# Kernel tuning notes

Hardware: AMD Instinct MI355X
Metric: run time of the kernel (lower is better)

## Reference

```python
import jax, jax.numpy as jnp
import numpy as np

N_NODES = 100000
N_EDGES = 1600000
IN_FEAT = 512
HIDDEN = 128
N_CLASSES = 7


def gcn_conv(x, edge_index, edge_weight, W, b):
    """PyG GCNConv: add self-loops (weight 1), symmetric normalization, linear, scatter-add, bias."""
    n = x.shape[0]
    src = jnp.concatenate([edge_index[0], jnp.arange(n, dtype=edge_index.dtype)])
    dst = jnp.concatenate([edge_index[1], jnp.arange(n, dtype=edge_index.dtype)])
    w = jnp.concatenate([edge_weight, jnp.ones((n,), dtype=edge_weight.dtype)])
    deg = jax.ops.segment_sum(w, dst, num_segments=n)  # degree on destination (col)
    dinv = jnp.where(deg > 0, jax.lax.rsqrt(deg), 0.0)
    norm = dinv[src] * w * dinv[dst]                   # [E+N]
    h = x @ W                                          # [N, out] transform BEFORE propagate
    msg = h[src] * norm[:, None]                       # [E+N, out] irregular gather
    out = jax.ops.segment_sum(msg, dst, num_segments=n)  # scatter-reduce
    return out + b


def setup_inputs() -> dict:
    key = jax.random.key(0)
    k1, k2, k3, k4, k5, k6 = jax.random.split(key, 6)
    x = jax.random.normal(k1, (N_NODES, IN_FEAT), dtype=jnp.float32)
    edge_index = jax.random.randint(k2, (2, N_EDGES), 0, N_NODES, dtype=jnp.int32)
    edge_weight = jax.random.uniform(k3, (N_EDGES,), dtype=jnp.float32)
    s1 = 1.0 / np.sqrt(IN_FEAT)
    s2 = 1.0 / np.sqrt(HIDDEN)
    W1 = jax.random.uniform(k4, (IN_FEAT, HIDDEN), dtype=jnp.float32, minval=-s1, maxval=s1)
    b1 = jnp.zeros((HIDDEN,), dtype=jnp.float32)
    W2 = jax.random.uniform(k5, (HIDDEN, N_CLASSES), dtype=jnp.float32, minval=-s2, maxval=s2)
    b2 = jnp.zeros((N_CLASSES,), dtype=jnp.float32)
    return {"x": x, "edge_index": edge_index, "edge_weight": edge_weight,
            "W1": W1, "b1": b1, "W2": W2, "b2": b2}


def reference(x, edge_index, edge_weight, W1, b1, W2, b2):
    # eval mode: F.dropout(training=False) is identity
    h = jax.nn.elu(gcn_conv(x, edge_index, edge_weight, W1, b1))
    out = gcn_conv(h, edge_index, edge_weight, W2, b2)
    return jax.nn.log_softmax(out, axis=1)
```

## Files before the change

### kernel.cpp

```cpp
#include <hip/hip_runtime.h>
#include <hip/hip_bf16.h>
#include <math.h>

#define N_NODES 100000
#define N_EDGES 1600000
#define IN_F 512
#define HID 128
#define NCLS 7

#define DEG_SHIFT 43
#define DEG_WMASK ((1ull << 43) - 1)
#define DEG_SCALE 4194304.0f
#define DEG_INV_SCALE (1.0f / 4194304.0f)

typedef short short8 __attribute__((ext_vector_type(8)));
typedef float f32x4 __attribute__((ext_vector_type(4)));

__device__ __forceinline__ unsigned pack_bf16x2(float a, float b) {
  unsigned ua = __float_as_uint(a), ub = __float_as_uint(b);
  unsigned ra = (ua + 0x7FFFu + ((ua >> 16) & 1u)) >> 16;
  unsigned rb = (ub + 0x7FFFu + ((ub >> 16) & 1u)) >> 16;
  return ra | (rb << 16);
}
__device__ __forceinline__ unsigned short f32_to_bf16(float v) {
  unsigned u = __float_as_uint(v);
  return (unsigned short)((u + 0x7FFFu + ((u >> 16) & 1u)) >> 16);
}
__device__ __forceinline__ float bf_lo(unsigned u) { return __uint_as_float(u << 16); }
__device__ __forceinline__ float bf_hi(unsigned u) { return __uint_as_float(u & 0xFFFF0000u); }

__global__ void k_deg_count(const int* __restrict__ ei, const float* __restrict__ ew,
                            unsigned long long* __restrict__ packed, int* __restrict__ rank) {
  int e = blockIdx.x * blockDim.x + threadIdx.x;
  if (e >= N_EDGES) return;
  int d = ei[N_EDGES + e];
  unsigned long long fx = (unsigned long long)(ew[e] * DEG_SCALE + 0.5f);
  unsigned long long old = atomicAdd(&packed[d], (1ull << DEG_SHIFT) | fx);
  rank[e] = (int)(old >> DEG_SHIFT);
}

__global__ void k_dinv(const unsigned long long* __restrict__ packed,
                       float* __restrict__ dinv, int* __restrict__ cnt,
                       uint2* __restrict__ csr_pad) {
  int i = blockIdx.x * blockDim.x + threadIdx.x;
  if (i < 8) csr_pad[i] = make_uint2(0u, 0u);
  if (i >= N_NODES) return;
  unsigned long long p = packed[i];
  cnt[i] = (int)(p >> DEG_SHIFT);
  float wsum = (float)(p & DEG_WMASK) * DEG_INV_SCALE;
  dinv[i] = rsqrtf(wsum + 1.0f);
}

__global__ void k_w1t(const float* __restrict__ W1, uint4* __restrict__ w1bf) {
  int idx = blockIdx.x * 256 + threadIdx.x;
  int lane = idx & 63;
  int st = idx >> 6;
  int t = st & 7, s = st >> 3;
  int n = t * 16 + (lane & 15);
  int k0 = s * 32 + (lane >> 4) * 8;
  uint4 v;
  v.x = pack_bf16x2(W1[(size_t)(k0 + 0) * HID + n], W1[(size_t)(k0 + 1) * HID + n]);
  v.y = pack_bf16x2(W1[(size_t)(k0 + 2) * HID + n], W1[(size_t)(k0 + 3) * HID + n]);
  v.z = pack_bf16x2(W1[(size_t)(k0 + 4) * HID + n], W1[(size_t)(k0 + 5) * HID + n]);
  v.w = pack_bf16x2(W1[(size_t)(k0 + 6) * HID + n], W1[(size_t)(k0 + 7) * HID + n]);
  w1bf[idx] = v;
}

__global__ void k_scan_partial(const int* __restrict__ cnt, int* __restrict__ bsum) {
  __shared__ int s[256];
  int t = threadIdx.x;
  int base = blockIdx.x * 1024;
  int v = 0;
#pragma unroll
  for (int q = 0; q < 4; q++) {
    int idx = base + t * 4 + q;
    if (idx < N_NODES) v += cnt[idx];
  }
  s[t] = v;
  __syncthreads();
  for (int o = 128; o > 0; o >>= 1) {
    if (t < o) s[t] += s[t + o];
    __syncthreads();
  }
  if (t == 0) bsum[blockIdx.x] = s[0];
}

__global__ void k_scan_bsum(int* bsum, int nb) {
  if (threadIdx.x == 0 && blockIdx.x == 0) {
    int acc = 0;
    for (int i = 0; i < nb; i++) { int v = bsum[i]; bsum[i] = acc; acc += v; }
  }
}

__global__ void k_scan_final(const int* __restrict__ cnt, const int* __restrict__ bsum,
                             int* __restrict__ offs) {
  __shared__ int s[256];
  int t = threadIdx.x;
  int base = blockIdx.x * 1024;
  int v[4]; int sum = 0;
#pragma unroll
  for (int q = 0; q < 4; q++) {
    int idx = base + t * 4 + q;
    v[q] = (idx < N_NODES) ? cnt[idx] : 0;
    sum += v[q];
  }
  s[t] = sum;
  __syncthreads();
  for (int o = 1; o < 256; o <<= 1) {
    int x = (t >= o) ? s[t - o] : 0;
    __syncthreads();
    s[t] += x;
    __syncthreads();
  }
  int acc = s[t] - sum + bsum[blockIdx.x];
#pragma unroll
  for (int q = 0; q < 4; q++) {
    int idx = base + t * 4 + q;
    if (idx < N_NODES) offs[idx] = acc;
    acc += v[q];
  }
}

__global__ void k_fill(const int* __restrict__ ei, const float* __restrict__ ew,
                       const int* __restrict__ rank, const int* __restrict__ offs,
                       uint2* __restrict__ csr) {
  int e = blockIdx.x * blockDim.x + threadIdx.x;
  if (e >= N_EDGES) return;
  int sidx = ei[e];
  int d = ei[N_EDGES + e];
  int p = offs[d] + rank[e];
  csr[p] = make_uint2((unsigned)sidx, __float_as_uint(ew[e]));
}

#define SLABSTRIDE 132
__global__ __launch_bounds__(256) void k_gemm1(const float* __restrict__ x,
                                               const uint4* __restrict__ w1bf,
                                               const float* __restrict__ dinv,
                                               unsigned short* __restrict__ h_u16) {
  __shared__ unsigned slab[4 * 16 * SLABSTRIDE];
  const int tid = threadIdx.x;
  const int lane = tid & 63;
  const int wv = tid >> 6;
  const int gw = blockIdx.x * 4 + wv;
  if (gw >= N_NODES / 16) return;
  const int m0 = gw * 16;
  unsigned* ws = slab + wv * 16 * SLABSTRIDE;
  const int l16 = lane & 15, quad = lane >> 4;

  f32x4 acc[8];
#pragma unroll
  for (int t = 0; t < 8; t++) acc[t] = (f32x4){0.f, 0.f, 0.f, 0.f};

#pragma unroll
  for (int hf = 0; hf < 2; hf++) {
#pragma unroll
    for (int b = 0; b < 2; b++) {
      float4 v[8];
#pragma unroll
      for (int i = 0; i < 8; i++) {
        int row = b * 8 + i;
        v[i] = *(const float4*)(x + (size_t)(m0 + row) * IN_F + hf * 256 + lane * 4);
      }
#pragma unroll
      for (int i = 0; i < 8; i++) {
        int row = b * 8 + i;
        unsigned lo = pack_bf16x2(v[i].x, v[i].y);
        unsigned hi = pack_bf16x2(v[i].z, v[i].w);
        *(uint2*)&ws[row * SLABSTRIDE + lane * 2] = make_uint2(lo, hi);
      }
    }
    __threadfence_block();
#pragma unroll
    for (int ks = 0; ks < 8; ks++) {
      short8 af = *(const short8*)&ws[l16 * SLABSTRIDE + ks * 16 + quad * 4];
      const uint4* bbase = w1bf + (size_t)(hf * 8 + ks) * 8 * 64 + lane;
#pragma unroll
      for (int t = 0; t < 8; t++) {
        uint4 bv = bbase[t * 64];
        acc[t] = __builtin_amdgcn_mfma_f32_16x16x32_bf16(af, *(const short8*)&bv,
                                                         acc[t], 0, 0, 0);
      }
    }
  }
  float df[4];
#pragma unroll
  for (int r = 0; r < 4; r++) df[r] = dinv[m0 + quad * 4 + r];
#pragma unroll
  for (int t = 0; t < 8; t++)
#pragma unroll
    for (int r = 0; r < 4; r++)
      h_u16[(size_t)(m0 + quad * 4 + r) * HID + t * 16 + l16] = f32_to_bf16(acc[t][r] * df[r]);
}

__global__ __launch_bounds__(256) void k_agg1(const unsigned* __restrict__ h_u,
    const float* __restrict__ dinv, const int* __restrict__ offs, const int* __restrict__ cnt,
    const uint2* __restrict__ csr, const float* __restrict__ b1,
    unsigned* __restrict__ act1_u) {
  int i = blockIdx.x * 4 + (threadIdx.x >> 6);
  int lane = threadIdx.x & 63;
  if (i >= N_NODES) return;
  int start = offs[i], len = cnt[i];
  int end = start + len;
  float ax = 0.f, ay = 0.f;
  for (int p = start; p < end; p += 8) {
    uint2 e[8];
#pragma unroll
    for (int k = 0; k < 8; k++) e[k] = csr[p + k];
    unsigned u[8];
#pragma unroll
    for (int k = 0; k < 8; k++) u[k] = h_u[(size_t)e[k].x * 64 + lane];
#pragma unroll
    for (int k = 0; k < 8; k++) {
      float n = (k == 0 || p + k < end) ? __uint_as_float(e[k].y) : 0.f;
      ax = fmaf(bf_lo(u[k]), n, ax);
      ay = fmaf(bf_hi(u[k]), n, ay);
    }
  }
  float di = dinv[i];
  unsigned u = h_u[(size_t)i * 64 + lane];
  float2 bb = *(const float2*)(b1 + lane * 2);
  float vx = fmaf(di, ax + bf_lo(u), bb.x);
  float vy = fmaf(di, ay + bf_hi(u), bb.y);
  vx = vx > 0.f ? vx : expm1f(vx);
  vy = vy > 0.f ? vy : expm1f(vy);
  act1_u[(size_t)i * 64 + lane] = pack_bf16x2(vx, vy);
}

__global__ __launch_bounds__(256) void k_gemm2(const unsigned* __restrict__ act1_u,
                                               const float* __restrict__ W2,
                                               const float* __restrict__ dinv,
                                               float* __restrict__ h2) {
  __shared__ float sA[32][HID + 1];
  __shared__ float sW[HID * NCLS];
  const int tid = threadIdx.x;
  const int r0 = blockIdx.x * 32;
#pragma unroll
  for (int j = 0; j < 8; j++) {
    int idx = tid + j * 256;
    int row = idx >> 6;
    int c = idx & 63;
    unsigned u = act1_u[(size_t)(r0 + row) * 64 + c];
    sA[row][c * 2]     = bf_lo(u);
    sA[row][c * 2 + 1] = bf_hi(u);
  }
#pragma unroll
  for (int j = 0; j < 4; j++) {
    int idx = tid + j * 256;
    if (idx < HID * NCLS) sW[idx] = W2[idx];
  }
  __syncthreads();
  const int r = tid >> 3;
  const int c = tid & 7;
  float acc = 0.0f;
  if (c < NCLS) {
#pragma unroll 8
    for (int k = 0; k < HID; k++) acc = fmaf(sA[r][k], sW[k * NCLS + c], acc);
  }
  h2[(size_t)(r0 + r) * 8 + c] = acc * dinv[r0 + r];
}

__global__ __launch_bounds__(256) void k_agg2(const float* __restrict__ h2,
    const float* __restrict__ dinv, const int* __restrict__ offs, const int* __restrict__ cnt,
    const uint2* __restrict__ csr, const float* __restrict__ b2, float* __restrict__ out) {
  int tid = threadIdx.x;
  int i = blockIdx.x * 32 + (tid >> 3);
  int f = tid & 7;
  if (i >= N_NODES) return;
  int start = offs[i], len = cnt[i];
  int end = start + len;
  float acc = 0.0f;
  for (int p = start; p < end; p += 4) {
    uint2 e0 = csr[p];
    uint2 e1 = csr[p + 1];
    uint2 e2 = csr[p + 2];
    uint2 e3 = csr[p + 3];
    float v0 = h2[(size_t)e0.x * 8 + f];
    float v1 = h2[(size_t)e1.x * 8 + f];
    float v2 = h2[(size_t)e2.x * 8 + f];
    float v3 = h2[(size_t)e3.x * 8 + f];
    float n0 = __uint_as_float(e0.y);
    float n1 = (p + 1 < end) ? __uint_as_float(e1.y) : 0.f;
    float n2 = (p + 2 < end) ? __uint_as_float(e2.y) : 0.f;
    float n3 = (p + 3 < end) ? __uint_as_float(e3.y) : 0.f;
    acc = fmaf(v0, n0, acc);
    acc = fmaf(v1, n1, acc);
    acc = fmaf(v2, n2, acc);
    acc = fmaf(v3, n3, acc);
  }
  float di = dinv[i];
  float v = fmaf(di, acc + h2[(size_t)i * 8 + f], (f < NCLS) ? b2[f] : 0.0f);
  float vm = (f < NCLS) ? v : -INFINITY;
#pragma unroll
  for (int o = 1; o < 8; o <<= 1) vm = fmaxf(vm, __shfl_xor(vm, o, 8));
  float ex = (f < NCLS) ? expf(v - vm) : 0.0f;
  float s8 = ex;
#pragma unroll
  for (int o = 1; o < 8; o <<= 1) s8 += __shfl_xor(s8, o, 8);
  float lse = logf(s8);
  if (f < NCLS) out[(size_t)i * NCLS + f] = v - vm - lse;
}

extern "C" void kernel_launch(void* const* d_in, const int* in_sizes, int n_in,
                              void* d_out, int out_size, void* d_ws, size_t ws_size,
                              hipStream_t stream) {
  const float* x  = (const float*)d_in[0];
  const int*   ei = (const int*)d_in[1];
  const float* ew = (const float*)d_in[2];
  const float* W1 = (const float*)d_in[3];
  const float* b1 = (const float*)d_in[4];
  const float* W2 = (const float*)d_in[5];
  const float* b2 = (const float*)d_in[6];
  float* out = (float*)d_out;

  char* w = (char*)d_ws;
  const size_t Npad  = ((size_t)N_NODES * 4 + 255) & ~(size_t)255;
  const size_t Npad8 = ((size_t)N_NODES * 8 + 255) & ~(size_t)255;
  const size_t Epad  = ((size_t)N_EDGES * 4 + 255) & ~(size_t)255;
  size_t off = 0;
  unsigned long long* packed = (unsigned long long*)(w + off); off += Npad8;
  float*    dinv     = (float*)(w + off);    off += Npad;
  int*      cnt      = (int*)(w + off);      off += Npad;
  int*      offs     = (int*)(w + off);      off += Npad;
  int*      bsum     = (int*)(w + off);      off += 1024;
  int*      rank     = (int*)(w + off);      off += Epad;
  uint2*    csr      = (uint2*)(w + off);    off += ((size_t)(N_EDGES + 8) * 8 + 255) & ~(size_t)255;
  uint4*    w1bf     = (uint4*)(w + off);    off += (size_t)8192 * 16;
  unsigned short* h_u16 = (unsigned short*)(w + off); off += (size_t)N_NODES * HID * 2;
  unsigned* act1_u   = (unsigned*)(w + off); off += (size_t)N_NODES * 64 * 4;
  float*    h2       = (float*)(w + off);    off += (size_t)N_NODES * 8 * 4;

  hipMemsetAsync(packed, 0, Npad8, stream);

  k_deg_count<<<N_EDGES / 256, 256, 0, stream>>>(ei, ew, packed, rank);
  k_w1t<<<32, 256, 0, stream>>>(W1, w1bf);
  k_dinv<<<(N_NODES + 255) / 256, 256, 0, stream>>>(packed, dinv, cnt, csr + N_EDGES);
  const int nb = (N_NODES + 1023) / 1024;
  k_scan_partial<<<nb, 256, 0, stream>>>(cnt, bsum);
  k_scan_bsum<<<1, 64, 0, stream>>>(bsum, nb);
  k_scan_final<<<nb, 256, 0, stream>>>(cnt, bsum, offs);
  k_fill<<<N_EDGES / 256, 256, 0, stream>>>(ei, ew, rank, offs, csr);
  const int g1_waves = N_NODES / 16;
  k_gemm1<<<(g1_waves + 3) / 4, 256, 0, stream>>>(x, w1bf, dinv, h_u16);
  k_agg1<<<(N_NODES + 3) / 4, 256, 0, stream>>>((const unsigned*)h_u16, dinv, offs, cnt,
                                                csr, b1, act1_u);
  k_gemm2<<<N_NODES / 32, 256, 0, stream>>>(act1_u, W2, dinv, h2);
  k_agg2<<<N_NODES / 32, 256, 0, stream>>>(h2, dinv, offs, cnt, csr, b2, out);
}
```

Measured before the change: 550.1 us.

## Fuse setup kernels, fold gemm2 into agg1, simplify CSR fill and gemm1

Merges the dinv, W1 bf16 transpose and partial-scan kernels into one launch. Drops the per-edge rank array in favour of atomic cursor slots during the CSR fill, and reuses the advanced cursor as the row end. Folds the 128x7 second GEMM into the first aggregation epilogue using a wave-wide shuffle reduction, which removes the act1 round trip. gemm1 now loads A fragments straight from global memory instead of staging them in LDS. agg2 assigns one wave per node with edge-parallel lanes. The atomic fill makes CSR order nondeterministic, so float summation order varies between runs.

New measurement: 641.4 us. 16.6% more time.

```diff
diff --git a/kernel.cpp b/kernel.cpp
--- a/kernel.cpp
+++ b/kernel.cpp
@@ -1,5 +1,4 @@
 #include <hip/hip_runtime.h>
-#include <hip/hip_bf16.h>
 #include <math.h>
 
 #define N_NODES 100000
@@ -12,6 +11,7 @@
 #define DEG_WMASK ((1ull << 43) - 1)
 #define DEG_SCALE 4194304.0f
 #define DEG_INV_SCALE (1.0f / 4194304.0f)
+#define NB_SCAN 98
 
 typedef short short8 __attribute__((ext_vector_type(8)));
 typedef float f32x4 __attribute__((ext_vector_type(4)));
@@ -29,60 +29,56 @@
 __device__ __forceinline__ float bf_lo(unsigned u) { return __uint_as_float(u << 16); }
 __device__ __forceinline__ float bf_hi(unsigned u) { return __uint_as_float(u & 0xFFFF0000u); }
 
-__global__ void k_deg_count(const int* __restrict__ ei, const float* __restrict__ ew,
-                            unsigned long long* __restrict__ packed, int* __restrict__ rank) {
-  int e = blockIdx.x * blockDim.x + threadIdx.x;
-  if (e >= N_EDGES) return;
+__global__ void k_deg(const int* __restrict__ ei, const float* __restrict__ ew,
+                      unsigned long long* __restrict__ packed) {
+  int e = blockIdx.x * 256 + threadIdx.x;
   int d = ei[N_EDGES + e];
   unsigned long long fx = (unsigned long long)(ew[e] * DEG_SCALE + 0.5f);
-  unsigned long long old = atomicAdd(&packed[d], (1ull << DEG_SHIFT) | fx);
-  rank[e] = (int)(old >> DEG_SHIFT);
-}
-
-__global__ void k_dinv(const unsigned long long* __restrict__ packed,
-                       float* __restrict__ dinv, int* __restrict__ cnt,
-                       uint2* __restrict__ csr_pad) {
-  int i = blockIdx.x * blockDim.x + threadIdx.x;
-  if (i < 8) csr_pad[i] = make_uint2(0u, 0u);
-  if (i >= N_NODES) return;
-  unsigned long long p = packed[i];
-  cnt[i] = (int)(p >> DEG_SHIFT);
-  float wsum = (float)(p & DEG_WMASK) * DEG_INV_SCALE;
-  dinv[i] = rsqrtf(wsum + 1.0f);
-}
-
-__global__ void k_w1t(const float* __restrict__ W1, uint4* __restrict__ w1bf) {
-  int idx = blockIdx.x * 256 + threadIdx.x;
-  int lane = idx & 63;
-  int st = idx >> 6;
-  int t = st & 7, s = st >> 3;
-  int n = t * 16 + (lane & 15);
-  int k0 = s * 32 + (lane >> 4) * 8;
-  uint4 v;
-  v.x = pack_bf16x2(W1[(size_t)(k0 + 0) * HID + n], W1[(size_t)(k0 + 1) * HID + n]);
-  v.y = pack_bf16x2(W1[(size_t)(k0 + 2) * HID + n], W1[(size_t)(k0 + 3) * HID + n]);
-  v.z = pack_bf16x2(W1[(size_t)(k0 + 4) * HID + n], W1[(size_t)(k0 + 5) * HID + n]);
-  v.w = pack_bf16x2(W1[(size_t)(k0 + 6) * HID + n], W1[(size_t)(k0 + 7) * HID + n]);
-  w1bf[idx] = v;
-}
-
-__global__ void k_scan_partial(const int* __restrict__ cnt, int* __restrict__ bsum) {
-  __shared__ int s[256];
-  int t = threadIdx.x;
-  int base = blockIdx.x * 1024;
+  atomicAdd(&packed[d], (1ull << DEG_SHIFT) | fx);
+}
+
+__global__ void k_mid(const unsigned long long* __restrict__ packed,
+                      float* __restrict__ dinv, int* __restrict__ cnt, int* __restrict__ bsum,
+                      const float* __restrict__ W1, uint4* __restrict__ w1bf,
+                      uint2* __restrict__ csr_pad) {
+  const int b = blockIdx.x, t = threadIdx.x;
+  if (b >= NB_SCAN) {
+    int idx = (b - NB_SCAN) * 256 + t;
+    if (idx < 8) csr_pad[idx] = make_uint2(0u, 0u);
+    int lane = idx & 63;
+    int st = idx >> 6;
+    int tt = st & 7, ss = st >> 3;
+    int n = tt * 16 + (lane & 15);
+    int k0 = ss * 32 + (lane >> 4) * 8;
+    uint4 v;
+    v.x = pack_bf16x2(W1[(size_t)(k0 + 0) * HID + n], W1[(size_t)(k0 + 1) * HID + n]);
+    v.y = pack_bf16x2(W1[(size_t)(k0 + 2) * HID + n], W1[(size_t)(k0 + 3) * HID + n]);
+    v.z = pack_bf16x2(W1[(size_t)(k0 + 4) * HID + n], W1[(size_t)(k0 + 5) * HID + n]);
+    v.w = pack_bf16x2(W1[(size_t)(k0 + 6) * HID + n], W1[(size_t)(k0 + 7) * HID + n]);
+    w1bf[idx] = v;
+    return;
+  }
+  __shared__ int sh[256];
+  int base = b * 1024;
   int v = 0;
 #pragma unroll
   for (int q = 0; q < 4; q++) {
     int idx = base + t * 4 + q;
-    if (idx < N_NODES) v += cnt[idx];
-  }
-  s[t] = v;
+    if (idx < N_NODES) {
+      unsigned long long p = packed[idx];
+      int c = (int)(p >> DEG_SHIFT);
+      cnt[idx] = c;
+      dinv[idx] = rsqrtf((float)(p & DEG_WMASK) * DEG_INV_SCALE + 1.0f);
+      v += c;
+    }
+  }
+  sh[t] = v;
   __syncthreads();
   for (int o = 128; o > 0; o >>= 1) {
-    if (t < o) s[t] += s[t + o];
+    if (t < o) sh[t] += sh[t + o];
     __syncthreads();
   }
-  if (t == 0) bsum[blockIdx.x] = s[0];
+  if (t == 0) bsum[b] = sh[0];
 }
 
 __global__ void k_scan_bsum(int* bsum, int nb) {
@@ -93,7 +89,7 @@
 }
 
 __global__ void k_scan_final(const int* __restrict__ cnt, const int* __restrict__ bsum,
-                             int* __restrict__ offs) {
+                             int* __restrict__ offs, int* __restrict__ cursor) {
   __shared__ int s[256];
   int t = threadIdx.x;
   int base = blockIdx.x * 1024;
@@ -116,70 +112,54 @@
 #pragma unroll
   for (int q = 0; q < 4; q++) {
     int idx = base + t * 4 + q;
-    if (idx < N_NODES) offs[idx] = acc;
+    if (idx < N_NODES) { offs[idx] = acc; cursor[idx] = acc; }
     acc += v[q];
   }
 }
 
 __global__ void k_fill(const int* __restrict__ ei, const float* __restrict__ ew,
-                       const int* __restrict__ rank, const int* __restrict__ offs,
-                       uint2* __restrict__ csr) {
-  int e = blockIdx.x * blockDim.x + threadIdx.x;
-  if (e >= N_EDGES) return;
-  int sidx = ei[e];
+                       int* __restrict__ cursor, uint2* __restrict__ csr) {
+  int e = blockIdx.x * 256 + threadIdx.x;
+  int s = ei[e];
   int d = ei[N_EDGES + e];
-  int p = offs[d] + rank[e];
-  csr[p] = make_uint2((unsigned)sidx, __float_as_uint(ew[e]));
-}
-
-#define SLABSTRIDE 132
+  int p = atomicAdd(&cursor[d], 1);
+  csr[p] = make_uint2((unsigned)s, __float_as_uint(ew[e]));
+}
+
 __global__ __launch_bounds__(256) void k_gemm1(const float* __restrict__ x,
                                                const uint4* __restrict__ w1bf,
                                                const float* __restrict__ dinv,
                                                unsigned short* __restrict__ h_u16) {
-  __shared__ unsigned slab[4 * 16 * SLABSTRIDE];
   const int tid = threadIdx.x;
   const int lane = tid & 63;
   const int wv = tid >> 6;
   const int gw = blockIdx.x * 4 + wv;
   if (gw >= N_NODES / 16) return;
   const int m0 = gw * 16;
-  unsigned* ws = slab + wv * 16 * SLABSTRIDE;
   const int l16 = lane & 15, quad = lane >> 4;
+  const float* arow = x + (size_t)(m0 + l16) * IN_F + quad * 8;
 
   f32x4 acc[8];
 #pragma unroll
   for (int t = 0; t < 8; t++) acc[t] = (f32x4){0.f, 0.f, 0.f, 0.f};
 
 #pragma unroll
-  for (int hf = 0; hf < 2; hf++) {
-#pragma unroll
-    for (int b = 0; b < 2; b++) {
-      float4 v[8];
-#pragma unroll
-      for (int i = 0; i < 8; i++) {
-        int row = b * 8 + i;
-        v[i] = *(const float4*)(x + (size_t)(m0 + row) * IN_F + hf * 256 + lane * 4);
-      }
-#pragma unroll
-      for (int i = 0; i < 8; i++) {
-        int row = b * 8 + i;
-        unsigned lo = pack_bf16x2(v[i].x, v[i].y);
-        unsigned hi = pack_bf16x2(v[i].z, v[i].w);
-        *(uint2*)&ws[row * SLABSTRIDE + lane * 2] = make_uint2(lo, hi);
-      }
-    }
-    __threadfence_block();
-#pragma unroll
-    for (int ks = 0; ks < 8; ks++) {
-      short8 af = *(const short8*)&ws[l16 * SLABSTRIDE + ks * 16 + quad * 4];
-      const uint4* bbase = w1bf + (size_t)(hf * 8 + ks) * 8 * 64 + lane;
-#pragma unroll
-      for (int t = 0; t < 8; t++) {
-        uint4 bv = bbase[t * 64];
-        acc[t] = __builtin_amdgcn_mfma_f32_16x16x32_bf16(af, *(const short8*)&bv,
-                                                         acc[t], 0, 0, 0);
-      }
+  for (int ks = 0; ks < 16; ks++) {
+    const float* ap = arow + ks * 32;
+    float4 a0 = *(const float4*)ap;
+    float4 a1 = *(const float4*)(ap + 4);
+    uint4 au;
+    au.x = pack_bf16x2(a0.x, a0.y);
+    au.y = pack_bf16x2(a0.z, a0.w);
+    au.z = pack_bf16x2(a1.x, a1.y);
+    au.w = pack_bf16x2(a1.z, a1.w);
+    short8 af = *(short8*)&au;
+    const uint4* bbase = w1bf + (size_t)ks * 8 * 64 + lane;
+#pragma unroll
+    for (int t = 0; t < 8; t++) {
+      uint4 bv = bbase[t * 64];
+      acc[t] = __builtin_amdgcn_mfma_f32_16x16x32_bf16(af, *(const short8*)&bv,
+                                                       acc[t], 0, 0, 0);
     }
   }
   float df[4];
@@ -193,14 +173,19 @@
 }
 
 __global__ __launch_bounds__(256) void k_agg1(const unsigned* __restrict__ h_u,
-    const float* __restrict__ dinv, const int* __restrict__ offs, const int* __restrict__ cnt,
+    const float* __restrict__ dinv, const int* __restrict__ offs, const int* __restrict__ ends,
     const uint2* __restrict__ csr, const float* __restrict__ b1,
-    unsigned* __restrict__ act1_u) {
+    const float* __restrict__ W2, float* __restrict__ h2) {
   int i = blockIdx.x * 4 + (threadIdx.x >> 6);
   int lane = threadIdx.x & 63;
   if (i >= N_NODES) return;
-  int start = offs[i], len = cnt[i];
-  int end = start + len;
+  float w2a[NCLS], w2b[NCLS];
+#pragma unroll
+  for (int c = 0; c < NCLS; c++) {
+    w2a[c] = W2[(size_t)(2 * lane) * NCLS + c];
+    w2b[c] = W2[(size_t)(2 * lane + 1) * NCLS + c];
+  }
+  int start = offs[i], end = ends[i];
   float ax = 0.f, ay = 0.f;
   for (int p = start; p < end; p += 8) {
     uint2 e[8];
@@ -223,81 +208,51 @@
   float vy = fmaf(di, ay + bf_hi(u), bb.y);
   vx = vx > 0.f ? vx : expm1f(vx);
   vy = vy > 0.f ? vy : expm1f(vy);
-  act1_u[(size_t)i * 64 + lane] = pack_bf16x2(vx, vy);
-}
-
-__global__ __launch_bounds__(256) void k_gemm2(const unsigned* __restrict__ act1_u,
-                                               const float* __restrict__ W2,
-                                               const float* __restrict__ dinv,
-                                               float* __restrict__ h2) {
-  __shared__ float sA[32][HID + 1];
-  __shared__ float sW[HID * NCLS];
-  const int tid = threadIdx.x;
-  const int r0 = blockIdx.x * 32;
-#pragma unroll
-  for (int j = 0; j < 8; j++) {
-    int idx = tid + j * 256;
-    int row = idx >> 6;
-    int c = idx & 63;
-    unsigned u = act1_u[(size_t)(r0 + row) * 64 + c];
-    sA[row][c * 2]     = bf_lo(u);
-    sA[row][c * 2 + 1] = bf_hi(u);
-  }
-#pragma unroll
-  for (int j = 0; j < 4; j++) {
-    int idx = tid + j * 256;
-    if (idx < HID * NCLS) sW[idx] = W2[idx];
-  }
-  __syncthreads();
-  const int r = tid >> 3;
-  const int c = tid & 7;
-  float acc = 0.0f;
-  if (c < NCLS) {
-#pragma unroll 8
-    for (int k = 0; k < HID; k++) acc = fmaf(sA[r][k], sW[k * NCLS + c], acc);
-  }
-  h2[(size_t)(r0 + r) * 8 + c] = acc * dinv[r0 + r];
+  float s[NCLS];
+#pragma unroll
+  for (int c = 0; c < NCLS; c++) s[c] = fmaf(vy, w2b[c], vx * w2a[c]);
+#pragma unroll
+  for (int m = 1; m < 64; m <<= 1) {
+#pragma unroll
+    for (int c = 0; c < NCLS; c++) s[c] += __shfl_xor(s[c], m);
+  }
+  if (lane < 8) {
+    float v = lane == 0 ? s[0] : lane == 1 ? s[1] : lane == 2 ? s[2] :
+              lane == 3 ? s[3] : lane == 4 ? s[4] : lane == 5 ? s[5] : s[6];
+    h2[(size_t)i * 8 + lane] = (lane < NCLS) ? v * di : 0.f;
+  }
 }
 
 __global__ __launch_bounds__(256) void k_agg2(const float* __restrict__ h2,
-    const float* __restrict__ dinv, const int* __restrict__ offs, const int* __restrict__ cnt,
+    const float* __restrict__ dinv, const int* __restrict__ offs, const int* __restrict__ ends,
     const uint2* __restrict__ csr, const float* __restrict__ b2, float* __restrict__ out) {
-  int tid = threadIdx.x;
-  int i = blockIdx.x * 32 + (tid >> 3);
-  int f = tid & 7;
+  int i = blockIdx.x * 4 + (threadIdx.x >> 6);
+  int lane = threadIdx.x & 63;
   if (i >= N_NODES) return;
-  int start = offs[i], len = cnt[i];
-  int end = start + len;
-  float acc = 0.0f;
-  for (int p = start; p < end; p += 4) {
-    uint2 e0 = csr[p];
-    uint2 e1 = csr[p + 1];
-    uint2 e2 = csr[p + 2];
-    uint2 e3 = csr[p + 3];
-    float v0 = h2[(size_t)e0.x * 8 + f];
-    float v1 = h2[(size_t)e1.x * 8 + f];
-    float v2 = h2[(size_t)e2.x * 8 + f];
-    float v3 = h2[(size_t)e3.x * 8 + f];
-    float n0 = __uint_as_float(e0.y);
-    float n1 = (p + 1 < end) ? __uint_as_float(e1.y) : 0.f;
-    float n2 = (p + 2 < end) ? __uint_as_float(e2.y) : 0.f;
-    float n3 = (p + 3 < end) ? __uint_as_float(e3.y) : 0.f;
-    acc = fmaf(v0, n0, acc);
-    acc = fmaf(v1, n1, acc);
-    acc = fmaf(v2, n2, acc);
-    acc = fmaf(v3, n3, acc);
-  }
+  int k = lane >> 3, f = lane & 7;
+  int start = offs[i], end = ends[i];
+  float acc = 0.f;
+  for (int p = start; p < end; p += 8) {
+    uint2 e = csr[p + k];
+    float n = (p + k < end) ? __uint_as_float(e.y) : 0.f;
+    acc = fmaf(h2[(size_t)e.x * 8 + f], n, acc);
+  }
+  acc += __shfl_xor(acc, 8);
+  acc += __shfl_xor(acc, 16);
+  acc += __shfl_xor(acc, 32);
   float di = dinv[i];
-  float v = fmaf(di, acc + h2[(size_t)i * 8 + f], (f < NCLS) ? b2[f] : 0.0f);
+  float v = fmaf(di, acc + h2[(size_t)i * 8 + f], (f < NCLS) ? b2[f] : 0.f);
   float vm = (f < NCLS) ? v : -INFINITY;
-#pragma unroll
-  for (int o = 1; o < 8; o <<= 1) vm = fmaxf(vm, __shfl_xor(vm, o, 8));
-  float ex = (f < NCLS) ? expf(v - vm) : 0.0f;
+  vm = fmaxf(vm, __shfl_xor(vm, 1));
+  vm = fmaxf(vm, __shfl_xor(vm, 2));
+  vm = fmaxf(vm, __shfl_xor(vm, 4));
+  float ex = (f < NCLS) ? expf(v - vm) : 0.f;
   float s8 = ex;
-#pragma unroll
-  for (int o = 1; o < 8; o <<= 1) s8 += __shfl_xor(s8, o, 8);
+  s8 += __shfl_xor(s8, 1);
+  s8 += __shfl_xor(s8, 2);
+  s8 += __shfl_xor(s8, 4);
   float lse = logf(s8);
-  if (f < NCLS) out[(size_t)i * NCLS + f] = v - vm - lse;
+  if (k == 0 && f < NCLS) out[(size_t)i * NCLS + f] = v - vm - lse;
 }
 
 extern "C" void kernel_launch(void* const* d_in, const int* in_sizes, int n_in,
@@ -315,34 +270,27 @@
   char* w = (char*)d_ws;
   const size_t Npad  = ((size_t)N_NODES * 4 + 255) & ~(size_t)255;
   const size_t Npad8 = ((size_t)N_NODES * 8 + 255) & ~(size_t)255;
-  const size_t Epad  = ((size_t)N_EDGES * 4 + 255) & ~(size_t)255;
   size_t off = 0;
   unsigned long long* packed = (unsigned long long*)(w + off); off += Npad8;
   float*    dinv     = (float*)(w + off);    off += Npad;
   int*      cnt      = (int*)(w + off);      off += Npad;
   int*      offs     = (int*)(w + off);      off += Npad;
+  int*      cursor   = (int*)(w + off);      off += Npad;
   int*      bsum     = (int*)(w + off);      off += 1024;
-  int*      rank     = (int*)(w + off);      off += Epad;
   uint2*    csr      = (uint2*)(w + off);    off += ((size_t)(N_EDGES + 8) * 8 + 255) & ~(size_t)255;
   uint4*    w1bf     = (uint4*)(w + off);    off += (size_t)8192 * 16;
   unsigned short* h_u16 = (unsigned short*)(w + off); off += (size_t)N_NODES * HID * 2;
-  unsigned* act1_u   = (unsigned*)(w + off); off += (size_t)N_NODES * 64 * 4;
   float*    h2       = (float*)(w + off);    off += (size_t)N_NODES * 8 * 4;
 
   hipMemsetAsync(packed, 0, Npad8, stream);
 
-  k_deg_count<<<N_EDGES / 256, 256, 0, stream>>>(ei, ew, packed, rank);
-  k_w1t<<<32, 256, 0, stream>>>(W1, w1bf);
-  k_dinv<<<(N_NODES + 255) / 256, 256, 0, stream>>>(packed, dinv, cnt, csr + N_EDGES);
-  const int nb = (N_NODES + 1023) / 1024;
-  k_scan_partial<<<nb, 256, 0, stream>>>(cnt, bsum);
-  k_scan_bsum<<<1, 64, 0, stream>>>(bsum, nb);
-  k_scan_final<<<nb, 256, 0, stream>>>(cnt, bsum, offs);
-  k_fill<<<N_EDGES / 256, 256, 0, stream>>>(ei, ew, rank, offs, csr);
-  const int g1_waves = N_NODES / 16;
-  k_gemm1<<<(g1_waves + 3) / 4, 256, 0, stream>>>(x, w1bf, dinv, h_u16);
-  k_agg1<<<(N_NODES + 3) / 4, 256, 0, stream>>>((const unsigned*)h_u16, dinv, offs, cnt,
-                                                csr, b1, act1_u);
-  k_gemm2<<<N_NODES / 32, 256, 0, stream>>>(act1_u, W2, dinv, h2);
-  k_agg2<<<N_NODES / 32, 256, 0, stream>>>(h2, dinv, offs, cnt, csr, b2, out);
-}
+  k_deg<<<N_EDGES / 256, 256, 0, stream>>>(ei, ew, packed);
+  k_mid<<<NB_SCAN + 32, 256, 0, stream>>>(packed, dinv, cnt, bsum, W1, w1bf, csr + N_EDGES);
+  k_scan_bsum<<<1, 64, 0, stream>>>(bsum, NB_SCAN);
+  k_scan_final<<<NB_SCAN, 256, 0, stream>>>(cnt, bsum, offs, cursor);
+  k_fill<<<N_EDGES / 256, 256, 0, stream>>>(ei, ew, cursor, csr);
+  k_gemm1<<<(N_NODES / 16 + 3) / 4, 256, 0, stream>>>(x, w1bf, dinv, h_u16);
+  k_agg1<<<(N_NODES + 3) / 4, 256, 0, stream>>>((const unsigned*)h_u16, dinv, offs, cursor,
+                                                csr, b1, W2, h2);
+  k_agg2<<<(N_NODES + 3) / 4, 256, 0, stream>>>(h2, dinv, offs, cursor, csr, b2, out);
+}
```
